# Kernel tuning notes

Hardware: AMD Instinct MI355X
Metric: run time of the kernel (lower is better)

Reference implementation:

```python
import jax, jax.numpy as jnp
import numpy as np
from jax import lax

KS = 3          # kernel_size
N = KS * KS     # number of sampling points
PAD = 1


def _conv2d(x, w, pad):
    # NCHW input, OIHW weights, stride 1
    return lax.conv_general_dilated(
        x, w, window_strides=(1, 1), padding=[(pad, pad), (pad, pad)],
        dimension_numbers=("NCHW", "OIHW", "NCHW"))


def setup_inputs() -> dict:
    key = jax.random.key(0)
    k1, k2, k3, k4 = jax.random.split(key, 4)
    x = jax.random.normal(k1, (8, 64, 128, 128), dtype=jnp.float32)
    w_conv = jax.random.normal(k2, (128, 64, 3, 3), dtype=jnp.float32) * 0.05
    # p_conv is zero-init in the original; use small random weights so offsets are
    # nonzero sub-pixel values and the bilinear path is exercised.
    w_p = jax.random.normal(k3, (2 * N, 64, 3, 3), dtype=jnp.float32) * 0.01
    b_p = jax.random.normal(k4, (2 * N,), dtype=jnp.float32) * 0.01
    return {"x": x, "w_conv": w_conv, "w_p": w_p, "b_p": b_p}


def reference(x, w_conv, w_p, b_p):
    b, c, H, W = x.shape
    # offset = p_conv(x): (b, 2N, H, W); first N channels are x (row) offsets,
    # last N are y (col) offsets
    offset = _conv2d(x, w_p, PAD) + b_p[None, :, None, None]

    x_pad = jnp.pad(x, ((0, 0), (0, 0), (PAD, PAD), (PAD, PAD)))
    Hp, Wp = H + 2 * PAD, W + 2 * PAD
    hi = jnp.float32(Hp - 1)  # original clamps BOTH coords with x.size(2)-1 (square)

    # p = p_0 (output-pixel coords) + p_n (kernel grid) + offset, as (b,H,W,2N)
    rng = jnp.arange(-(KS - 1) // 2, (KS - 1) // 2 + 1, dtype=jnp.float32)
    pnx, pny = jnp.meshgrid(rng, rng, indexing="ij")
    p_n = jnp.concatenate([pnx.ravel(), pny.ravel()])  # (2N,)
    p0x = jnp.arange(H, dtype=jnp.float32)[:, None, None] * jnp.ones((1, W, N), jnp.float32)
    p0y = jnp.arange(W, dtype=jnp.float32)[None, :, None] * jnp.ones((H, 1, N), jnp.float32)
    p_0 = jnp.concatenate([p0x, p0y], axis=-1)  # (H,W,2N)
    p = p_0[None] + p_n[None, None, None, :] + offset.transpose(0, 2, 3, 1)  # (b,H,W,2N)

    q_lt = jnp.floor(lax.stop_gradient(p))
    q_rb = q_lt + 1.0
    q_lt = jnp.clip(q_lt, 0.0, hi)
    q_rb = jnp.clip(q_rb, 0.0, hi)
    q_lb = jnp.concatenate([q_lt[..., :N], q_rb[..., N:]], axis=-1)
    q_rt = jnp.concatenate([q_rb[..., :N], q_lt[..., N:]], axis=-1)
    p = jnp.clip(p, 0.0, hi)

    px, py = p[..., :N], p[..., N:]
    g_lt = (1 + (q_lt[..., :N] - px)) * (1 + (q_lt[..., N:] - py))
    g_rb = (1 - (q_rb[..., :N] - px)) * (1 - (q_rb[..., N:] - py))
    g_lb = (1 + (q_lb[..., :N] - px)) * (1 - (q_lb[..., N:] - py))
    g_rt = (1 - (q_rt[..., :N] - px)) * (1 + (q_rt[..., N:] - py))

    flat = x_pad.reshape(b, c, Hp * Wp)

    def gather(q):  # q: (b,H,W,2N) -> (b,c,H,W,N)
        qi = q.astype(jnp.int32)
        idx = (qi[..., :N] * Wp + qi[..., N:]).reshape(b, -1)  # (b, H*W*N)
        g = jnp.take_along_axis(flat, jnp.broadcast_to(idx[:, None, :], (b, c, idx.shape[1])), axis=2)
        return g.reshape(b, c, H, W, N)

    x_off = (g_lt[:, None] * gather(q_lt) + g_rb[:, None] * gather(q_rb)
             + g_lb[:, None] * gather(q_lb) + g_rt[:, None] * gather(q_rt))  # (b,c,H,W,N)

    # final ks x ks conv over the sampled points == contraction over (c, N)
    outc = w_conv.shape[0]
    out = jnp.einsum("bchwn,ocn->bohw", x_off, w_conv.reshape(outc, c, N))
    return out
```

## Files before the change

### kernel.cpp

```cpp
#include <hip/hip_runtime.h>


#define HW    16384
#define CIN   64
#define OC    128

constexpr int WT_OFF   = 0;
constexpr int WP_OFF   = 11520;
constexpr int OFF_OFF  = WP_OFF + 73728;
constexpr int OFF_HALF = 8 * 9 * HW * 2;
constexpr int XT_OFF   = OFF_OFF + 2 * OFF_HALF;

__device__ __forceinline__ float clamp129(float v) {
  return fminf(fmaxf(v, 0.f), 129.f);
}

__device__ __forceinline__ void bilin_params(int row, int col, int n,
                                             float ox, float oy,
                                             float4& g, int4& idx) {
  float px = (float)(row + n / 3 - 1) + ox;
  float py = (float)(col + n % 3 - 1) + oy;
  float fx = floorf(px), fy = floorf(py);
  float qltx = clamp129(fx),       qlty = clamp129(fy);
  float qrbx = clamp129(fx + 1.f), qrby = clamp129(fy + 1.f);
  float pcx = clamp129(px),        pcy = clamp129(py);
  float dltx = 1.f + qltx - pcx, dlty = 1.f + qlty - pcy;
  float drbx = 1.f - qrbx + pcx, drby = 1.f - qrby + pcy;
  float gg[4] = {dltx * dlty, drbx * drby, dltx * drby, drbx * dlty};
  int rr[4]   = {(int)qltx, (int)qrbx, (int)qltx, (int)qrbx};
  int cc[4]   = {(int)qlty, (int)qrby, (int)qrby, (int)qlty};
  int ii[4];
#pragma unroll
  for (int k = 0; k < 4; ++k) {
    bool v = (rr[k] >= 1) && (rr[k] <= 128) && (cc[k] >= 1) && (cc[k] <= 128);
    ii[k] = v ? ((rr[k] - 1) * 128 + (cc[k] - 1)) : 0;
    if (!v) gg[k] = 0.f;
  }
  g   = make_float4(gg[0], gg[1], gg[2], gg[3]);
  idx = make_int4(ii[0], ii[1], ii[2], ii[3]);
}

__global__ __launch_bounds__(256) void repack_kernel(
    const float* __restrict__ w_conv, const float* __restrict__ w_p,
    float* __restrict__ wP, float* __restrict__ wT) {
  int i = blockIdx.x * 256 + threadIdx.x;
  if (i < 73728) {
    int o = i & 127, m = i >> 7, n = m >> 6, c = m & 63;
    wP[i] = w_conv[o * 576 + c * 9 + n];
  }
  int j = i - 73728;
  if (j >= 0 && j < 11520) {
    int m = j / 20, n2 = j - m * 20;
    wT[j] = (n2 < 18) ? w_p[n2 * 576 + m] : 0.f;
  }
}

__global__ __launch_bounds__(256) void transpose_kernel(
    const float* __restrict__ x, float* __restrict__ xT) {
  __shared__ float t[64][65];
  const int b   = blockIdx.y;
  const int hw0 = blockIdx.x * 64;
  const int tid = threadIdx.x;
  {
    const int hwi = tid & 63, cq = tid >> 6;
    const float* xb = x + b * (CIN * HW);
#pragma unroll
    for (int k = 0; k < 16; ++k) {
      int c = cq * 16 + k;
      t[hwi][c] = xb[c * HW + hw0 + hwi];
    }
  }
  __syncthreads();
  {
    const int ci = tid & 63, hq = tid >> 6;
    float* xTb = xT + ((size_t)b * HW + hw0) * CIN;
#pragma unroll
    for (int k = 0; k < 16; ++k) {
      int hwi = hq * 16 + k;
      xTb[hwi * CIN + ci] = t[hwi][ci];
    }
  }
}

__global__ __launch_bounds__(256) void offs_kernel(
    const float* __restrict__ x, const float* __restrict__ wT,
    float* __restrict__ offp) {
  const int half = blockIdx.z;
  const int b    = blockIdx.y;
  const int hw   = blockIdx.x * 256 + threadIdx.x;
  const int row  = hw >> 7;
  const int w    = hw & 127;

  float acc[18];
#pragma unroll
  for (int i = 0; i < 18; ++i) acc[i] = 0.f;

  const float* xb = x + b * (CIN * HW);
  const int c0 = half * 32;
  for (int ci = c0; ci < c0 + 32; ++ci) {
    const float* xs = xb + ci * HW;
#pragma unroll
    for (int kh = 0; kh < 3; ++kh) {
      int r = row + kh - 1;
      bool vr = (unsigned)r < 128u;
      int base = r * 128 + w;
      float rbv[3];
      rbv[0] = (vr && w >= 1)   ? xs[base - 1] : 0.f;
      rbv[1] = vr               ? xs[base]     : 0.f;
      rbv[2] = (vr && w <= 126) ? xs[base + 1] : 0.f;
#pragma unroll
      for (int kw = 0; kw < 3; ++kw) {
        const float* wr = wT + (ci * 9 + kh * 3 + kw) * 20;
        float xv = rbv[kw];
#pragma unroll
        for (int n2 = 0; n2 < 18; ++n2)
          acc[n2] = fmaf(xv, wr[n2], acc[n2]);
      }
    }
  }

  float* dst = offp + half * OFF_HALF;
#pragma unroll
  for (int n = 0; n < 9; ++n) {
    *(float2*)(dst + ((b * 9 + n) * HW + hw) * 2) =
        make_float2(acc[n], acc[n + 9]);
  }
}

__global__ __launch_bounds__(256) void main_kernel(
    const float* __restrict__ xT, const float* __restrict__ wP,
    const float* __restrict__ offp, const float* __restrict__ b_p,
    float* __restrict__ out) {
  __shared__ __align__(16) float xlds[8 * 576];

  const int b    = blockIdx.y;
  const int px0  = blockIdx.x * 64;
  const int tid  = threadIdx.x;
  const int lane = tid & 63;
  const bool has3 = (tid < 64);

  const int ow_u = __builtin_amdgcn_readfirstlane((tid >> 6) * 32);
  const float* __restrict__ wPu = wP + ow_u;

  float4 g0, g1, g2 = make_float4(0.f, 0.f, 0.f, 0.f);
  int4   i0, i1, i2 = make_int4(0, 0, 0, 0);
  {
    const float* oh0 = offp;
    const float* oh1 = offp + OFF_HALF;
#pragma unroll
    for (int j = 0; j < 3; ++j) {
      if (j == 2 && !has3) break;
      int t = tid + j * 256;
      int n = t >> 6, hw = px0 + (t & 63);
      int oidx = ((b * 9 + n) * HW + hw) * 2;
      float2 pa = *(const float2*)(oh0 + oidx);
      float2 pb = *(const float2*)(oh1 + oidx);
      float ox = pa.x + pb.x + b_p[n];
      float oy = pa.y + pb.y + b_p[n + 9];
      float4 g; int4 ii;
      bilin_params(hw >> 7, hw & 127, n, ox, oy, g, ii);
      if (j == 0) { g0 = g; i0 = ii; }
      else if (j == 1) { g1 = g; i1 = ii; }
      else { g2 = g; i2 = ii; }
    }
  }

  float acc[32];
#pragma unroll
  for (int k = 0; k < 32; ++k) acc[k] = 0.f;

  const float* xTb = xT + (size_t)b * HW * CIN;

#define GATH(G, I, POS)                                                    \
  {                                                                        \
    const float* pa = xTb + (I).x * CIN + c0;                              \
    const float* pb = xTb + (I).y * CIN + c0;                              \
    const float* pc = xTb + (I).z * CIN + c0;                              \
    const float* pd = xTb + (I).w * CIN + c0;                              \
    float4 A0 = *(const float4*)pa, A1 = *(const float4*)(pa + 4);         \
    float4 B0 = *(const float4*)pb, B1 = *(const float4*)(pb + 4);         \
    float4 C0 = *(const float4*)pc, C1 = *(const float4*)(pc + 4);         \
    float4 D0 = *(const float4*)pd, D1 = *(const float4*)(pd + 4);         \
    float* dst = xlds + (POS);                                             \
    dst[0 * 576] = (G).x*A0.x + (G).y*B0.x + (G).z*C0.x + (G).w*D0.x;      \
    dst[1 * 576] = (G).x*A0.y + (G).y*B0.y + (G).z*C0.y + (G).w*D0.y;      \
    dst[2 * 576] = (G).x*A0.z + (G).y*B0.z + (G).z*C0.z + (G).w*D0.z;      \
    dst[3 * 576] = (G).x*A0.w + (G).y*B0.w + (G).z*C0.w + (G).w*D0.w;      \
    dst[4 * 576] = (G).x*A1.x + (G).y*B1.x + (G).z*C1.x + (G).w*D1.x;      \
    dst[5 * 576] = (G).x*A1.y + (G).y*B1.y + (G).z*C1.y + (G).w*D1.y;      \
    dst[6 * 576] = (G).x*A1.z + (G).y*B1.z + (G).z*C1.z + (G).w*D1.z;      \
    dst[7 * 576] = (G).x*A1.w + (G).y*B1.w + (G).z*C1.w + (G).w*D1.w;      \
  }

  for (int cc = 0; cc < 8; ++cc) {
    const int c0 = cc * 8;
    __syncthreads();
    GATH(g0, i0, tid);
    GATH(g1, i1, tid + 256);
    if (has3) GATH(g2, i2, tid + 512);
    __syncthreads();
#pragma unroll
    for (int c = 0; c < 8; ++c) {
      const int cg = c0 + c;
#pragma unroll
      for (int n = 0; n < 9; ++n) {
        float xv = xlds[c * 576 + n * 64 + lane];
        const float* wr = wPu + (n * 64 + cg) * 128;
#pragma unroll
        for (int k = 0; k < 32; ++k)
          acc[k] = fmaf(wr[k], xv, acc[k]);
      }
    }
  }
#undef GATH

#pragma unroll
  for (int k = 0; k < 32; ++k) {
    out[((size_t)b * OC + ow_u + k) * HW + px0 + lane] = acc[k];
  }
}

extern "C" void kernel_launch(void* const* d_in, const int* in_sizes, int n_in,
                              void* d_out, int out_size, void* d_ws, size_t ws_size,
                              hipStream_t stream) {
  const float* x      = (const float*)d_in[0];
  const float* w_conv = (const float*)d_in[1];
  const float* w_p    = (const float*)d_in[2];
  const float* b_p    = (const float*)d_in[3];
  float* outp = (float*)d_out;
  float* ws   = (float*)d_ws;

  float* wT   = ws + WT_OFF;
  float* wP   = ws + WP_OFF;
  float* offp = ws + OFF_OFF;
  float* xT   = ws + XT_OFF;

  repack_kernel<<<333, 256, 0, stream>>>(w_conv, w_p, wP, wT);
  transpose_kernel<<<dim3(256, 8), 256, 0, stream>>>(x, xT);
  offs_kernel<<<dim3(64, 8, 2), 256, 0, stream>>>(x, wT, offp);
  main_kernel<<<dim3(256, 8), 256, 0, stream>>>(xT, wP, offp, b_p, outp);
}
```

Measured before the change: 479.9 us.

## Prefetch next channel chunk of bilinear gathers into registers during FMA loop

Main kernel now processes channels in chunks of 4 instead of 8. It issues the global gather loads for the next chunk into registers before running the FMA loop on the current chunk in LDS, then reduces and writes them to LDS after a barrier. The goal is to hide gather latency behind compute. It halves the LDS footprint but doubles the number of barrier rounds and keeps 48 extra float registers live, which may lower occupancy.

```diff
diff --git a/kernel.cpp b/kernel.cpp
--- a/kernel.cpp
+++ b/kernel.cpp
@@ -127,11 +127,29 @@
   }
 }
 
+struct C4 { float4 a, b, c, d; };
+
+__device__ __forceinline__ void gload(const float* __restrict__ xTb,
+                                      const int4& I, int c0, C4& L) {
+  L.a = *(const float4*)(xTb + I.x * CIN + c0);
+  L.b = *(const float4*)(xTb + I.y * CIN + c0);
+  L.c = *(const float4*)(xTb + I.z * CIN + c0);
+  L.d = *(const float4*)(xTb + I.w * CIN + c0);
+}
+
+__device__ __forceinline__ void redw(const C4& L, const float4& G,
+                                     float* __restrict__ dst) {
+  dst[0]    = G.x * L.a.x + G.y * L.b.x + G.z * L.c.x + G.w * L.d.x;
+  dst[576]  = G.x * L.a.y + G.y * L.b.y + G.z * L.c.y + G.w * L.d.y;
+  dst[1152] = G.x * L.a.z + G.y * L.b.z + G.z * L.c.z + G.w * L.d.z;
+  dst[1728] = G.x * L.a.w + G.y * L.b.w + G.z * L.c.w + G.w * L.d.w;
+}
+
 __global__ __launch_bounds__(256) void main_kernel(
     const float* __restrict__ xT, const float* __restrict__ wP,
     const float* __restrict__ offp, const float* __restrict__ b_p,
     float* __restrict__ out) {
-  __shared__ __align__(16) float xlds[8 * 576];
+  __shared__ __align__(16) float xlds[4 * 576];
 
   const int b    = blockIdx.y;
   const int px0  = blockIdx.x * 64;
@@ -171,37 +189,25 @@
 
   const float* xTb = xT + (size_t)b * HW * CIN;
 
-#define GATH(G, I, POS)                                                    \
-  {                                                                        \
-    const float* pa = xTb + (I).x * CIN + c0;                              \
-    const float* pb = xTb + (I).y * CIN + c0;                              \
-    const float* pc = xTb + (I).z * CIN + c0;                              \
-    const float* pd = xTb + (I).w * CIN + c0;                              \
-    float4 A0 = *(const float4*)pa, A1 = *(const float4*)(pa + 4);         \
-    float4 B0 = *(const float4*)pb, B1 = *(const float4*)(pb + 4);         \
-    float4 C0 = *(const float4*)pc, C1 = *(const float4*)(pc + 4);         \
-    float4 D0 = *(const float4*)pd, D1 = *(const float4*)(pd + 4);         \
-    float* dst = xlds + (POS);                                             \
-    dst[0 * 576] = (G).x*A0.x + (G).y*B0.x + (G).z*C0.x + (G).w*D0.x;      \
-    dst[1 * 576] = (G).x*A0.y + (G).y*B0.y + (G).z*C0.y + (G).w*D0.y;      \
-    dst[2 * 576] = (G).x*A0.z + (G).y*B0.z + (G).z*C0.z + (G).w*D0.z;      \
-    dst[3 * 576] = (G).x*A0.w + (G).y*B0.w + (G).z*C0.w + (G).w*D0.w;      \
-    dst[4 * 576] = (G).x*A1.x + (G).y*B1.x + (G).z*C1.x + (G).w*D1.x;      \
-    dst[5 * 576] = (G).x*A1.y + (G).y*B1.y + (G).z*C1.y + (G).w*D1.y;      \
-    dst[6 * 576] = (G).x*A1.z + (G).y*B1.z + (G).z*C1.z + (G).w*D1.z;      \
-    dst[7 * 576] = (G).x*A1.w + (G).y*B1.w + (G).z*C1.w + (G).w*D1.w;      \
-  }
-
-  for (int cc = 0; cc < 8; ++cc) {
-    const int c0 = cc * 8;
+  C4 L0, L1, L2;
+  gload(xTb, i0, 0, L0);
+  gload(xTb, i1, 0, L1);
+  if (has3) gload(xTb, i2, 0, L2);
+  redw(L0, g0, xlds + tid);
+  redw(L1, g1, xlds + tid + 256);
+  if (has3) redw(L2, g2, xlds + tid + 512);
+
+  for (int cc = 0; cc < 16; ++cc) {
     __syncthreads();
-    GATH(g0, i0, tid);
-    GATH(g1, i1, tid + 256);
-    if (has3) GATH(g2, i2, tid + 512);
-    __syncthreads();
-#pragma unroll
-    for (int c = 0; c < 8; ++c) {
-      const int cg = c0 + c;
+    if (cc < 15) {
+      const int c0n = (cc + 1) * 4;
+      gload(xTb, i0, c0n, L0);
+      gload(xTb, i1, c0n, L1);
+      if (has3) gload(xTb, i2, c0n, L2);
+    }
+#pragma unroll
+    for (int c = 0; c < 4; ++c) {
+      const int cg = cc * 4 + c;
 #pragma unroll
       for (int n = 0; n < 9; ++n) {
         float xv = xlds[c * 576 + n * 64 + lane];
@@ -211,8 +217,13 @@
           acc[k] = fmaf(wr[k], xv, acc[k]);
       }
     }
-  }
-#undef GATH
+    __syncthreads();
+    if (cc < 15) {
+      redw(L0, g0, xlds + tid);
+      redw(L1, g1, xlds + tid + 256);
+      if (has3) redw(L2, g2, xlds + tid + 512);
+    }
+  }
 
 #pragma unroll
   for (int k = 0; k < 32; ++k) {
```

Result: slower. 1.507 ms (+214.0%).
